# Kernel optimization log

Measured on AMD Instinct MI355X. Metric: run time of the kernel, lower is better.

## Reference

```python
import jax, jax.numpy as jnp
import numpy as np

C, N, NC, E, D, R = 16, 10000, 2000, 50000, 256, 32
NBLK = 3
IN_DIM = 4 + 134 + 6 * 4 + 18 * 4  # 234
EPS = 1e-5


def _instance_norm(x):
    # InstanceNorm1d (affine=False): normalize over the node axis per (config, channel)
    mu = jnp.mean(x, axis=1, keepdims=True)
    var = jnp.var(x, axis=1, keepdims=True)
    return (x - mu) * jax.lax.rsqrt(var + EPS)


def _channel_attn(x, W1, b1, W2, b2):
    t = jax.nn.relu(x @ W1 + b1)
    return jax.nn.sigmoid(t @ W2 + b2) * x


def setup_inputs() -> dict:
    key = jax.random.key(0)
    ks = jax.random.split(key, 24)
    sc = 0.05
    inp = {}
    inp["x_node_cfg"] = jax.random.randint(ks[0], (C, NC, 18), 0, 6)
    inp["x_feat"] = jax.random.normal(ks[1], (N, 134), jnp.float32)
    inp["x_node_layout_feat"] = jax.random.randint(ks[2], (N, 6), 0, 6)
    inp["x_op"] = jax.random.randint(ks[3], (N,), 0, 120)
    inp["edge_index"] = jax.random.randint(ks[4], (2, E), 0, N)
    inp["node_config_ids"] = jnp.arange(NC)
    # parameters
    inp["emb_op"] = jax.random.normal(ks[5], (120, 4)) * 0.1
    inp["emb_layout"] = jax.random.normal(ks[6], (8, 4)) * 0.1
    inp["lin1_W"] = jax.random.normal(ks[7], (IN_DIM, D)) * sc
    inp["lin1_b"] = jnp.full((D,), 0.01, jnp.float32)
    inp["ca1_W1"] = jax.random.normal(ks[8], (D, R)) * sc
    inp["ca1_b1"] = jnp.zeros((R,), jnp.float32)
    inp["ca1_W2"] = jax.random.normal(ks[9], (R, D)) * sc
    inp["ca1_b2"] = jnp.zeros((D,), jnp.float32)
    inp["lin2_W"] = jax.random.normal(ks[10], (D, D)) * sc
    inp["lin2_b"] = jnp.full((D,), 0.01, jnp.float32)
    inp["ca2_W1"] = jax.random.normal(ks[11], (D, R)) * sc
    inp["ca2_b1"] = jnp.zeros((R,), jnp.float32)
    inp["ca2_W2"] = jax.random.normal(ks[12], (R, D)) * sc
    inp["ca2_b2"] = jnp.zeros((D,), jnp.float32)
    inp["sage_Wl"] = jax.random.normal(ks[13], (NBLK, D, D)) * sc
    inp["sage_bl"] = jnp.zeros((NBLK, D), jnp.float32)
    inp["sage_Wr"] = jax.random.normal(ks[14], (NBLK, D, D)) * sc
    inp["sca_W1"] = jax.random.normal(ks[15], (NBLK, D, R)) * sc
    inp["sca_b1"] = jnp.zeros((NBLK, R), jnp.float32)
    inp["sca_W2"] = jax.random.normal(ks[16], (NBLK, R, D)) * sc
    inp["sca_b2"] = jnp.zeros((NBLK, D), jnp.float32)
    inp["cls_W"] = jax.random.normal(ks[17], (D, 1)) * sc
    inp["cls_b"] = jnp.zeros((1,), jnp.float32)
    return inp


def _forward(x_node_cfg, x_feat, x_node_layout_feat, x_op, edge_index, node_config_ids,
             emb_op, emb_layout, lin1_W, lin1_b, ca1_W1, ca1_b1, ca1_W2, ca1_b2,
             lin2_W, lin2_b, ca2_W1, ca2_b1, ca2_W2, ca2_b2,
             sage_Wl, sage_bl, sage_Wr, sca_W1, sca_b1, sca_W2, sca_b2, cls_W, cls_b):
    n_cfg = x_node_cfg.shape[0]
    n_nodes = x_feat.shape[0]
    # build per-node config feature: -2 fill, scatter configured nodes, shift by +2
    node_cfg = jnp.full((n_cfg, n_nodes, 18), -2, x_node_cfg.dtype)
    node_cfg = node_cfg.at[:, node_config_ids].set(x_node_cfg) + 2
    cfg_emb = emb_layout[node_cfg].reshape(n_cfg, n_nodes, 18 * 4)  # [C,N,72]
    layout_emb = emb_layout[x_node_layout_feat + 2].reshape(n_nodes, 6 * 4)  # [N,24]
    op_emb = emb_op[x_op]  # [N,4]
    feat = jnp.concatenate([
        jnp.broadcast_to(x_feat[None], (n_cfg, n_nodes, x_feat.shape[1])),
        cfg_emb,
        jnp.broadcast_to(layout_emb[None], (n_cfg, n_nodes, layout_emb.shape[1])),
        jnp.broadcast_to(op_emb[None], (n_cfg, n_nodes, op_emb.shape[1])),
    ], axis=2)  # [C,N,234]

    # LinearActNorm 1
    h = feat @ lin1_W + lin1_b
    h = _instance_norm(h)
    h = _channel_attn(h, ca1_W1, ca1_b1, ca1_W2, ca1_b2)
    h = jax.nn.gelu(h, approximate=False)
    # LinearActNorm 2
    h = h @ lin2_W + lin2_b
    h = _instance_norm(h)
    h = _channel_attn(h, ca2_W1, ca2_b1, ca2_W2, ca2_b2)
    h = jax.nn.gelu(h, approximate=False)

    src, tgt = edge_index[0], edge_index[1]
    cnt = jnp.zeros((n_nodes,), h.dtype).at[tgt].add(1.0)
    inv_cnt = (1.0 / jnp.maximum(cnt, 1.0))[None, :, None]
    for i in range(sage_Wl.shape[0]):
        shortcut = h
        x = _instance_norm(h)
        # SAGEConv: mean aggregation of source features at targets + root transform
        agg = jnp.zeros_like(x).at[:, tgt, :].add(x[:, src, :]) * inv_cnt
        x = agg @ sage_Wl[i] + sage_bl[i] + x @ sage_Wr[i]
        x = _channel_attn(x, sca_W1[i], sca_b1[i], sca_W2[i], sca_b2[i])
        h = jax.nn.gelu(x + shortcut, approximate=False)

    pooled = h.mean(axis=1)  # [C,D]
    return (pooled @ cls_W + cls_b).reshape(-1)  # [C]


def reference(x_node_cfg, x_feat, x_node_layout_feat, x_op, edge_index, node_config_ids,
              emb_op, emb_layout, lin1_W, lin1_b, ca1_W1, ca1_b1, ca1_W2, ca1_b2,
              lin2_W, lin2_b, ca2_W1, ca2_b1, ca2_W2, ca2_b2,
              sage_Wl, sage_bl, sage_Wr, sca_W1, sca_b1, sca_W2, sca_b2, cls_W, cls_b):
    return _forward(x_node_cfg, x_feat, x_node_layout_feat, x_op, edge_index, node_config_ids,
                    emb_op, emb_layout, lin1_W, lin1_b, ca1_W1, ca1_b1, ca1_W2, ca1_b2,
                    lin2_W, lin2_b, ca2_W1, ca2_b1, ca2_W2, ca2_b2,
                    sage_Wl, sage_bl, sage_Wr, sca_W1, sca_b1, sca_W2, sca_b2, cls_W, cls_b)
```

## Files before the change

### kernel.cpp

```cpp
#include <hip/hip_runtime.h>
#include <hip/hip_bf16.h>
#include <math.h>

constexpr int C_  = 16;
constexpr int N_  = 10000;
constexpr int NC_ = 2000;
constexpr int E_  = 50000;
constexpr int D_  = 256;
constexpr int SZ_ = N_ * D_;
constexpr float EPS_ = 1e-5f;

typedef unsigned short u16;
typedef __attribute__((ext_vector_type(8))) unsigned short us8v;
typedef __attribute__((ext_vector_type(4))) unsigned short us4v;
typedef __attribute__((ext_vector_type(8))) short s16x8;
typedef __attribute__((ext_vector_type(4))) float f32x4;

typedef __attribute__((address_space(3))) unsigned int lds_uint;
typedef const __attribute__((address_space(1))) unsigned int glb_uint;

__device__ __forceinline__ u16 f2bf(float f) {
    __hip_bfloat16 h = __float2bfloat16(f);
    return __builtin_bit_cast(u16, h);
}
__device__ __forceinline__ float bf2f(u16 h) {
    return __uint_as_float(((unsigned)h) << 16);
}
__device__ __forceinline__ float gelu_f(float x) {
    float z = x * 0.70710678118654752f;
    float az = fabsf(z);
    float t = 1.f / fmaf(0.3275911f, az, 1.f);
    float p = t * (0.254829592f + t * (-0.284496736f + t * (1.421413741f +
              t * (-1.453152027f + t * 1.061405429f))));
    float e = p * __expf(-z * z);
    float erfv = (z >= 0.f) ? (1.f - e) : (e - 1.f);
    return 0.5f * x * (1.f + erfv);
}


__global__ __launch_bounds__(256) void tbl_k(const float* __restrict__ embL,
                                             const float* __restrict__ W,
                                             float* __restrict__ T) {
    int b = blockIdx.x;
    int s = b >> 3, i = b & 7, d = threadIdx.x;
    float acc = 0.f;
#pragma unroll
    for (int k = 0; k < 4; ++k)
        acc = fmaf(embL[i * 4 + k], W[(134 + s * 4 + k) * 256 + d], acc);
    T[(s * 8 + i) * 256 + d] = acc;
}

__global__ __launch_bounds__(256) void csum_k(const float* __restrict__ T,
                                              float* __restrict__ cs) {
    int d = threadIdx.x;
    float a = 0.f;
#pragma unroll
    for (int s = 0; s < 18; ++s) a += T[(s * 8) * 256 + d];
    cs[d] = a;
}

__global__ __launch_bounds__(192) void feat_k(const float* __restrict__ xf,
                                              const int* __restrict__ xlay,
                                              const int* __restrict__ xop,
                                              const float* __restrict__ embL,
                                              const float* __restrict__ embO,
                                              float* __restrict__ f) {
    int n = blockIdx.x, j = threadIdx.x;
    if (j >= 176) return;
    float v;
    if (j < 134) v = xf[n * 134 + j];
    else if (j < 158) { int q = j - 134; int t = q >> 2, k = q & 3; v = embL[(xlay[n * 6 + t] + 2) * 4 + k]; }
    else if (j < 162) { int k = j - 158; v = embO[xop[n] * 4 + k]; }
    else v = 0.f;
    f[n * 176 + j] = v;
}

__global__ __launch_bounds__(256) void wpack_k(const float* __restrict__ W,
                                               float* __restrict__ Wp) {
    int j = blockIdx.x, d = threadIdx.x;
    float v = 0.f;
    if (j < 134) v = W[j * 256 + d];
    else if (j < 158) v = W[(206 + j - 134) * 256 + d];
    else if (j < 162) v = W[(230 + j - 158) * 256 + d];
    Wp[j * 256 + d] = v;
}

__global__ __launch_bounds__(256) void packw1_k(const float* __restrict__ W1,
                                                u16* __restrict__ dst) {
    int i = blockIdx.x * 256 + threadIdx.x;
    int j = i & 7, lane = (i >> 3) & 63, half = (i >> 9) & 1, ks = (i >> 10) & 1, wid = (i >> 11) & 3;
    int k = wid * 64 + ks * 32 + ((lane >> 4) << 3) + j;
    int col = half * 16 + (lane & 15);
    dst[i] = f2bf(W1[k * 32 + col]);
}
__global__ __launch_bounds__(256) void packw2_k(const float* __restrict__ W2,
                                                u16* __restrict__ dst) {
    int i = blockIdx.x * 256 + threadIdx.x;
    int j = i & 7, lane = (i >> 3) & 63, q = (i >> 9) & 3, wid = (i >> 11) & 3;
    int kq = lane >> 4, cl = lane & 15;
    dst[i] = f2bf(W2[(kq * 8 + j) * 256 + (wid * 4 + q) * 16 + cl]);
}

__global__ __launch_bounds__(256) void cfgpos_k(const int* __restrict__ ncid,
                                                int* __restrict__ cfgpos) {
    int i = blockIdx.x * 256 + threadIdx.x;
    if (i < NC_) cfgpos[ncid[i]] = i;
}

__global__ __launch_bounds__(256) void hist_k(const int* __restrict__ ei, int* __restrict__ cnt) {
    int e = blockIdx.x * 256 + threadIdx.x;
    if (e < E_) atomicAdd(&cnt[ei[E_ + e]], 1);
}

__global__ __launch_bounds__(1024) void scan_k(const int* __restrict__ cnt,
                                               int* __restrict__ off,
                                               int* __restrict__ cursor,
                                               float* __restrict__ invcnt) {
    __shared__ int s[1024];
    int t = threadIdx.x;
    int base = t * 10;
    int local[10];
    int part = 0;
#pragma unroll
    for (int k = 0; k < 10; ++k) {
        int idx = base + k;
        int v = (idx < N_) ? cnt[idx] : 0;
        local[k] = v; part += v;
    }
    s[t] = part;
    __syncthreads();
    for (int o = 1; o < 1024; o <<= 1) {
        int val = (t >= o) ? s[t - o] : 0;
        __syncthreads();
        s[t] += val;
        __syncthreads();
    }
    int pre = s[t] - part;
#pragma unroll
    for (int k = 0; k < 10; ++k) {
        int idx = base + k;
        if (idx < N_) {
            off[idx] = pre;
            cursor[idx] = pre;
            invcnt[idx] = 1.0f / (float)(local[k] > 1 ? local[k] : 1);
            pre += local[k];
        }
    }
    if (t == 1023) off[N_] = s[1023];
}

__global__ __launch_bounds__(256) void fill_k(const int* __restrict__ ei,
                                              int* __restrict__ cursor,
                                              int* __restrict__ csr) {
    int e = blockIdx.x * 256 + threadIdx.x;
    if (e < E_) {
        int t = ei[E_ + e];
        int p = atomicAdd(&cursor[t], 1);
        csr[p] = ei[e];
    }
}

__global__ __launch_bounds__(256) void wt2_k(const float* __restrict__ W,
                                             u16* __restrict__ Wt) {
    int j = blockIdx.x, k = threadIdx.x;
    Wt[j * 256 + k] = f2bf(W[k * 256 + j]);
}

__global__ __launch_bounds__(256) void foldw_k(const float* __restrict__ Wl,
                                               const float* __restrict__ Wr,
                                               const float* __restrict__ bl,
                                               const float* __restrict__ mu,
                                               const float* __restrict__ rs,
                                               u16* __restrict__ Wt,
                                               float* __restrict__ biasF) {
    __shared__ float red[256];
    int c = blockIdx.y, j = blockIdx.x, k = threadIdx.x;
    float rsv = rs[c * 256 + k], muv = mu[c * 256 + k];
    float fl = rsv * Wl[k * 256 + j];
    float fr = rsv * Wr[k * 256 + j];
    size_t wb = ((size_t)c * 256 + j) * 512;
    Wt[wb + k] = f2bf(fl);
    Wt[wb + 256 + k] = f2bf(fr);
    red[k] = muv * (fl + fr);
    __syncthreads();
    for (int s = 128; s > 0; s >>= 1) {
        if (k < s) red[k] += red[k + s];
        __syncthreads();
    }
    if (k == 0) biasF[c * 256 + j] = bl[j] - red[0];
}

__global__ __launch_bounds__(256) void lin1_cfg_k(const float* __restrict__ base,
                                                  const float* __restrict__ T,
                                                  const int* __restrict__ ncid,
                                                  const int* __restrict__ xcfg,
                                                  u16* __restrict__ H,
                                                  float* __restrict__ ssum,
                                                  float* __restrict__ ssq) {
    __shared__ int idxs[16][18];
    __shared__ int nid[16];
    const int c = blockIdx.z, j0 = blockIdx.x * 16, tid = threadIdx.x;
    if (tid < 16) nid[tid] = ncid[j0 + tid];
    for (int t = tid; t < 288; t += 256) {
        int row = t / 18, s = t - row * 18;
        idxs[row][s] = (xcfg[((size_t)c * NC_ + j0 + row) * 18 + s] + 2) * 256;
    }
    __syncthreads();
    const int d = tid;
    float psum = 0.f, psq = 0.f;
    for (int g = 0; g < 16; g += 4) {
        float acc[4];
#pragma unroll
        for (int gg = 0; gg < 4; ++gg) acc[gg] = base[(size_t)nid[g + gg] * 256 + d];
#pragma unroll
        for (int s = 0; s < 18; ++s) {
            const float* Ts = &T[s * 2048 + d];
#pragma unroll
            for (int gg = 0; gg < 4; ++gg)
                acc[gg] += Ts[idxs[g + gg][s]];
        }
#pragma unroll
        for (int gg = 0; gg < 4; ++gg) {
            H[((size_t)c * N_ + nid[g + gg]) * 256 + d] = f2bf(acc[gg]);
            psum += acc[gg]; psq += acc[gg] * acc[gg];
        }
    }
    atomicAdd(&ssum[c * 256 + d], psum);
    atomicAdd(&ssq[c * 256 + d], psq);
}

__global__ __launch_bounds__(256) void lin1_unc_k(const float* __restrict__ base,
                                                  const float* __restrict__ csum,
                                                  const int* __restrict__ cfgpos,
                                                  int nc,
                                                  u16* __restrict__ H,
                                                  float* __restrict__ ssum,
                                                  float* __restrict__ ssq) {
    __shared__ float red[2048];
    const int n0 = blockIdx.x * 16, tid = threadIdx.x;
    float ps[8] = {0, 0, 0, 0, 0, 0, 0, 0}, pq[8] = {0, 0, 0, 0, 0, 0, 0, 0};
#pragma unroll
    for (int it = 0; it < 2; ++it) {
        const int flat = tid + it * 256;
        const int row = flat >> 5, cb = (flat & 31) * 8;
        const int n = n0 + row;
        if (cfgpos[n] >= 0) continue;
        us8v b;
#pragma unroll
        for (int j = 0; j < 8; ++j) {
            float v = base[(size_t)n * 256 + cb + j] + csum[cb + j];
            b[j] = f2bf(v);
            ps[j] += v; pq[j] += v * v;
        }
        for (int c = 0; c < nc; ++c)
            *(us8v*)&H[((size_t)c * N_ + n) * 256 + cb] = b;
    }
#pragma unroll
    for (int j = 0; j < 8; ++j)
        red[((tid >> 5) * 32 + (tid & 31)) * 8 + j] = ps[j];
    __syncthreads();
    {
        const int cb2 = tid >> 3, j2 = tid & 7;
        float s = 0.f;
#pragma unroll
        for (int r8 = 0; r8 < 8; ++r8) s += red[(r8 * 32 + cb2) * 8 + j2];
        for (int c = 0; c < nc; ++c) atomicAdd(&ssum[c * 256 + tid], s);
    }
    __syncthreads();
#pragma unroll
    for (int j = 0; j < 8; ++j)
        red[((tid >> 5) * 32 + (tid & 31)) * 8 + j] = pq[j];
    __syncthreads();
    {
        const int cb2 = tid >> 3, j2 = tid & 7;
        float s = 0.f;
#pragma unroll
        for (int r8 = 0; r8 < 8; ++r8) s += red[(r8 * 32 + cb2) * 8 + j2];
        for (int c = 0; c < nc; ++c) atomicAdd(&ssq[c * 256 + tid], s);
    }
}

__global__ __launch_bounds__(256) void finstat_k(const float* __restrict__ ssum,
                                                 const float* __restrict__ ssq,
                                                 float* __restrict__ mu,
                                                 float* __restrict__ rs,
                                                 float* __restrict__ mrs) {
    int i = blockIdx.x * 256 + threadIdx.x;
    float m = ssum[i] * (1.0f / (float)N_);
    float v = ssq[i] * (1.0f / (float)N_) - m * m;
    float r = rsqrtf(v + EPS_);
    mu[i] = m;
    rs[i] = r;
    mrs[i] = m * r;
}

__global__ __launch_bounds__(256) void agg_k(const u16* __restrict__ H,
                                             const int* __restrict__ off,
                                             const int* __restrict__ csr,
                                             const float* __restrict__ invcnt,
                                             const float* __restrict__ mu,
                                             u16* __restrict__ Agg) {
    int wave = threadIdx.x >> 6, lane = threadIdx.x & 63;
    int pair = blockIdx.x * 4 + wave;
    int c = pair / N_, t = pair - c * N_;
    int d4 = lane * 4;
    int o0 = off[t], o1 = off[t + 1];
    int deg = o1 - o0;
    us4v o;
    if (deg > 0) {
        int myidx = (lane < deg) ? csr[o0 + lane] : 0;
        const u16* Hc = H + (size_t)c * SZ_ + d4;
        float ax = 0.f, ay = 0.f, az = 0.f, aw = 0.f;
        int lim = deg < 64 ? deg : 64;
        int i = 0;
        for (; i + 4 <= lim; i += 4) {
            int s0 = __shfl(myidx, i), s1 = __shfl(myidx, i + 1);
            int s2 = __shfl(myidx, i + 2), s3 = __shfl(myidx, i + 3);
            us4v h0 = *(const us4v*)&Hc[(size_t)s0 * 256];
            us4v h1 = *(const us4v*)&Hc[(size_t)s1 * 256];
            us4v h2 = *(const us4v*)&Hc[(size_t)s2 * 256];
            us4v h3 = *(const us4v*)&Hc[(size_t)s3 * 256];
            ax += (bf2f(h0.x) + bf2f(h1.x)) + (bf2f(h2.x) + bf2f(h3.x));
            ay += (bf2f(h0.y) + bf2f(h1.y)) + (bf2f(h2.y) + bf2f(h3.y));
            az += (bf2f(h0.z) + bf2f(h1.z)) + (bf2f(h2.z) + bf2f(h3.z));
            aw += (bf2f(h0.w) + bf2f(h1.w)) + (bf2f(h2.w) + bf2f(h3.w));
        }
        for (; i < lim; ++i) {
            int s = __shfl(myidx, i);
            us4v h = *(const us4v*)&Hc[(size_t)s * 256];
            ax += bf2f(h.x); ay += bf2f(h.y); az += bf2f(h.z); aw += bf2f(h.w);
        }
        for (int j = o0 + 64; j < o1; ++j) {
            int s = csr[j];
            us4v h = *(const us4v*)&Hc[(size_t)s * 256];
            ax += bf2f(h.x); ay += bf2f(h.y); az += bf2f(h.z); aw += bf2f(h.w);
        }
        float inv = invcnt[t];
        o.x = f2bf(ax * inv); o.y = f2bf(ay * inv);
        o.z = f2bf(az * inv); o.w = f2bf(aw * inv);
    } else {
        o.x = f2bf(mu[c * 256 + d4 + 0]);
        o.y = f2bf(mu[c * 256 + d4 + 1]);
        o.z = f2bf(mu[c * 256 + d4 + 2]);
        o.w = f2bf(mu[c * 256 + d4 + 3]);
    }
    *(us4v*)&Agg[((size_t)c * N_ + t) * 256 + d4] = o;
}

template <int STATS>
__global__ __launch_bounds__(256) void mgemm_k(
    const u16* __restrict__ A1, size_t sA1,
    const u16* __restrict__ A2, size_t sA2,
    const u16* __restrict__ Wt, size_t sW, int K1, int Ktot,
    const float* __restrict__ bias, size_t sBias,
    u16* __restrict__ Y, size_t sY, int Mrows,
    float* __restrict__ ssum, float* __restrict__ ssq)
{
    __shared__ u16 Asm[128 * 64];
    __shared__ u16 Bsm[128 * 64];
    const int tid = threadIdx.x;
    const int lane = tid & 63, wid = tid >> 6;
    const int wr = wid >> 1, wc = wid & 1;

    const int gx = gridDim.x, gy = gridDim.y;
    int nwg = gx * gy * gridDim.z;
    int orig = blockIdx.x + gx * (blockIdx.y + gy * blockIdx.z);
    int q = nwg >> 3, r = nwg & 7;
    int xcd = orig & 7, idx = orig >> 3;
    int swz = (xcd < r ? xcd * (q + 1) : r * (q + 1) + (xcd - r) * q) + idx;
    const int bx = swz % gx;
    const int tmp = swz / gx;
    const int by = tmp % gy;
    const int c  = tmp / gy;

    const int rowbase = by * 128, colbase = bx * 128;

    const u16* A1p = A1 + (size_t)c * sA1;
    const u16* A2p = A2 ? (A2 + (size_t)c * sA2) : nullptr;
    const u16* Wp  = Wt + (size_t)c * sW;

    f32x4 acc[4][4];
#pragma unroll
    for (int i = 0; i < 4; ++i)
#pragma unroll
        for (int j = 0; j < 4; ++j) acc[i][j] = (f32x4)0.f;

    const int lrow = lane >> 3;
    const int lchunk = lane & 7;

    for (int k0 = 0; k0 < Ktot; k0 += 64) {
        const u16* asrc; int ak;
        if (k0 < K1) { asrc = A1p; ak = k0; } else { asrc = A2p; ak = k0 - K1; }
#pragma unroll
        for (int i = 0; i < 4; ++i) {
            const int row = (wid * 4 + i) * 8 + lrow;
            const int srcchunk = lchunk ^ (row & 7);
            int garow = rowbase + row;
            if (garow >= Mrows) garow = Mrows - 1;
            const u16* ga = asrc + (size_t)garow * 256 + ak + srcchunk * 8;
            __builtin_amdgcn_global_load_lds((glb_uint*)ga,
                (lds_uint*)(Asm + (wid * 4 + i) * 512), 16, 0, 0);
            const u16* gb = Wp + (size_t)(colbase + row) * Ktot + k0 + srcchunk * 8;
            __builtin_amdgcn_global_load_lds((glb_uint*)gb,
                (lds_uint*)(Bsm + (wid * 4 + i) * 512), 16, 0, 0);
        }
        __syncthreads();
#pragma unroll
        for (int ks = 0; ks < 2; ++ks) {
            s16x8 aF[4], bF[4];
            const int kk = ks * 32 + ((lane >> 4) << 3);
#pragma unroll
            for (int f = 0; f < 4; ++f) {
                int ar = wr * 64 + f * 16 + (lane & 15);
                aF[f] = *(const s16x8*)&Asm[(ar * 64 + kk) ^ ((ar & 7) << 3)];
                int br = wc * 64 + f * 16 + (lane & 15);
                bF[f] = *(const s16x8*)&Bsm[(br * 64 + kk) ^ ((br & 7) << 3)];
            }
#pragma unroll
            for (int fr = 0; fr < 4; ++fr)
#pragma unroll
                for (int fc = 0; fc < 4; ++fc)
                    acc[fr][fc] = __builtin_amdgcn_mfma_f32_16x16x32_bf16(
                        aF[fr], bF[fc], acc[fr][fc], 0, 0, 0);
        }
        __syncthreads();
    }

    float bcol[4];
#pragma unroll
    for (int fc = 0; fc < 4; ++fc)
        bcol[fc] = bias[(size_t)c * sBias + colbase + wc * 64 + fc * 16 + (lane & 15)];
    u16* Yp = Y + (size_t)c * sY;
    float ps[4] = {0, 0, 0, 0}, pq[4] = {0, 0, 0, 0};
#pragma unroll
    for (int fr = 0; fr < 4; ++fr) {
#pragma unroll
        for (int i = 0; i < 4; ++i) {
            int grow = rowbase + wr * 64 + fr * 16 + ((lane >> 4) << 2) + i;
            if (grow < Mrows) {
                size_t rb = (size_t)grow * 256 + colbase + wc * 64 + (lane & 15);
#pragma unroll
                for (int fc = 0; fc < 4; ++fc) {
                    float v = acc[fr][fc][i] + bcol[fc];
                    Yp[rb + fc * 16] = f2bf(v);
                    if (STATS) { ps[fc] += v; pq[fc] += v * v; }
                }
            }
        }
    }
    if (STATS) {
#pragma unroll
        for (int fc = 0; fc < 4; ++fc) {
            float s = ps[fc], q2 = pq[fc];
            s += __shfl_xor(s, 16); s += __shfl_xor(s, 32);
            q2 += __shfl_xor(q2, 16); q2 += __shfl_xor(q2, 32);
            if (lane < 16) {
                int col = colbase + wc * 64 + fc * 16 + lane;
                atomicAdd(&ssum[c * 256 + col], s);
                atomicAdd(&ssq[c * 256 + col], q2);
            }
        }
    }
}

__global__ __launch_bounds__(256) void gemm_k(const float* __restrict__ A1, int lda1,
                                              const float* __restrict__ W1, int K1,
                                              const float* __restrict__ bias,
                                              float* __restrict__ Y, int Mrows) {
    __shared__ float As[16][132];
    __shared__ float Bs[16][132];
    float acc[8][8];
#pragma unroll
    for (int i = 0; i < 8; ++i)
#pragma unroll
        for (int j = 0; j < 8; ++j) acc[i][j] = 0.f;

    const int tid = threadIdx.x;
    const int tr = tid >> 4, tc = tid & 15;
    const int rowbase = blockIdx.y * 128, colbase = blockIdx.x * 128;

    for (int k0 = 0; k0 < K1; k0 += 16) {
#pragma unroll
        for (int ii = 0; ii < 2; ++ii) {
            int i = tid + ii * 256;
            int rr = i >> 2, qq = i & 3;
            int grow = rowbase + rr;
            float4 vv = make_float4(0.f, 0.f, 0.f, 0.f);
            if (grow < Mrows) vv = *(const float4*)&A1[(size_t)grow * lda1 + k0 + qq * 4];
            As[qq * 4 + 0][rr] = vv.x;
            As[qq * 4 + 1][rr] = vv.y;
            As[qq * 4 + 2][rr] = vv.z;
            As[qq * 4 + 3][rr] = vv.w;
        }
#pragma unroll
        for (int ii = 0; ii < 2; ++ii) {
            int i = tid + ii * 256;
            int rr = i >> 5, qq = i & 31;
            float4 vv = *(const float4*)&W1[(size_t)(k0 + rr) * 256 + colbase + qq * 4];
            *(float4*)&Bs[rr][qq * 4] = vv;
        }
        __syncthreads();
#pragma unroll
        for (int kk = 0; kk < 16; ++kk) {
            float a[8], b[8];
            *(float4*)&a[0] = *(const float4*)&As[kk][tr * 4];
            *(float4*)&a[4] = *(const float4*)&As[kk][64 + tr * 4];
            *(float4*)&b[0] = *(const float4*)&Bs[kk][tc * 4];
            *(float4*)&b[4] = *(const float4*)&Bs[kk][64 + tc * 4];
#pragma unroll
            for (int i = 0; i < 8; ++i)
#pragma unroll
                for (int j = 0; j < 8; ++j)
                    acc[i][j] = fmaf(a[i], b[j], acc[i][j]);
        }
        __syncthreads();
    }

    float4 blo = *(const float4*)&bias[colbase + tc * 4];
    float4 bhi = *(const float4*)&bias[colbase + 64 + tc * 4];
    float bb[8] = {blo.x, blo.y, blo.z, blo.w, bhi.x, bhi.y, bhi.z, bhi.w};
#pragma unroll
    for (int i = 0; i < 8; ++i)
#pragma unroll
        for (int j = 0; j < 8; ++j) acc[i][j] += bb[j];

#pragma unroll
    for (int i = 0; i < 8; ++i) {
        int lrow = (i < 4) ? (tr * 4 + i) : (64 + tr * 4 + (i - 4));
        int grow = rowbase + lrow;
        if (grow < Mrows) {
            *(float4*)&Y[(size_t)grow * 256 + colbase + tc * 4] =
                make_float4(acc[i][0], acc[i][1], acc[i][2], acc[i][3]);
            *(float4*)&Y[(size_t)grow * 256 + colbase + 64 + tc * 4] =
                make_float4(acc[i][4], acc[i][5], acc[i][6], acc[i][7]);
        }
    }
}

template <int NORM, int RES, int SMODE>
__global__ __launch_bounds__(512) void apply_k(const u16* __restrict__ Yin,
                                               u16* __restrict__ Hout,
                                               const u16* __restrict__ Hsc,
                                               const u16* __restrict__ W1p,
                                               const float* __restrict__ b1,
                                               const u16* __restrict__ W2p,
                                               const float* __restrict__ b2,
                                               const float* __restrict__ rs,
                                               const float* __restrict__ mrs,
                                               float* __restrict__ ssum,
                                               float* __restrict__ ssq) {
    __shared__ u16 vbf[16 * 264];
    __shared__ u16 scs[(RES ? 16 : 1) * 264];
    __shared__ float tpart[8 * 528];
    __shared__ u16 tbf[16 * 40];
    __shared__ float srs[NORM ? 256 : 1], smrs[NORM ? 256 : 1];
    const int c = blockIdx.z, n0 = blockIdx.x * 16, tid = threadIdx.x;
    const int lane = tid & 63, wid = tid >> 6;
    const size_t rowbase = ((size_t)c * N_ + n0) * 256;

    if (NORM && tid < 256) { srs[tid] = rs[c * 256 + tid]; smrs[tid] = mrs[c * 256 + tid]; }
    {
        const int row = tid >> 5, cb = (tid & 31) * 8;
        us8v x = *(const us8v*)&Yin[rowbase + row * 256 + cb];
        us8v r;
        if (RES) r = *(const us8v*)&Hsc[rowbase + row * 256 + cb];
        if (NORM) {
            __syncthreads();
            us8v y;
#pragma unroll
            for (int j = 0; j < 8; ++j)
                y[j] = f2bf(fmaf(bf2f(x[j]), srs[cb + j], -smrs[cb + j]));
            *(us8v*)&vbf[row * 264 + cb] = y;
        } else {
            *(us8v*)&vbf[row * 264 + cb] = x;
        }
        if (RES) *(us8v*)&scs[row * 264 + cb] = r;
    }
    __syncthreads();

    {
        const int arow = lane & 15, kq = lane >> 4;
        const int k = wid * 32 + kq * 8;
        s16x8 aF = *(const s16x8*)&vbf[arow * 264 + k];
        s16x8 bF0 = *(const s16x8*)&W1p[((wid * 2 + 0) * 64 + lane) * 8];
        s16x8 bF1 = *(const s16x8*)&W1p[((wid * 2 + 1) * 64 + lane) * 8];
        f32x4 at0 = __builtin_amdgcn_mfma_f32_16x16x32_bf16(aF, bF0, (f32x4)0.f, 0, 0, 0);
        f32x4 at1 = __builtin_amdgcn_mfma_f32_16x16x32_bf16(aF, bF1, (f32x4)0.f, 0, 0, 0);
#pragma unroll
        for (int i = 0; i < 4; ++i) {
            tpart[wid * 528 + (kq * 4 + i) * 33 + (lane & 15)] = at0[i];
            tpart[wid * 528 + (kq * 4 + i) * 33 + 16 + (lane & 15)] = at1[i];
        }
    }
    __syncthreads();

    {
        const int nr = tid >> 5, col = tid & 31;
        float s = b1[col];
#pragma unroll
        for (int w8 = 0; w8 < 8; ++w8)
            s += tpart[w8 * 528 + nr * 33 + col];
        tbf[nr * 40 + col] = f2bf(fmaxf(s, 0.f));
    }
    __syncthreads();

    {
        const int cl = lane & 15, kq = lane >> 4;
        s16x8 aF = *(const s16x8*)&tbf[cl * 40 + kq * 8];
        float ps[2] = {0, 0}, pq[2] = {0, 0};
#pragma unroll
        for (int q = 0; q < 2; ++q) {
            const int colb = (wid * 2 + q) * 16;
            s16x8 bF = *(const s16x8*)&W2p[((wid * 2 + q) * 64 + lane) * 8];
            f32x4 acc = __builtin_amdgcn_mfma_f32_16x16x32_bf16(aF, bF, (f32x4)0.f, 0, 0, 0);
            const float b2v = b2[colb + cl];
#pragma unroll
            for (int i = 0; i < 4; ++i) {
                const int row = kq * 4 + i;
                const int ea = row * 264 + colb + cl;
                float s = acc[i] + b2v;
                float sig = 1.0f / (1.0f + __expf(-s));
                float val = sig * bf2f(vbf[ea]);
                if (RES) val += bf2f(scs[ea]);
                val = gelu_f(val);
                vbf[ea] = f2bf(val);
                if (SMODE) { ps[q] += val; if (SMODE == 1) pq[q] += val * val; }
            }
        }
        if (SMODE) {
#pragma unroll
            for (int q = 0; q < 2; ++q) {
                float s = ps[q];
                s += __shfl_xor(s, 16); s += __shfl_xor(s, 32);
                if (SMODE == 1) {
                    float q2 = pq[q];
                    q2 += __shfl_xor(q2, 16); q2 += __shfl_xor(q2, 32);
                    if (lane < 16) atomicAdd(&ssq[c * 256 + (wid * 2 + q) * 16 + lane], q2);
                }
                if (lane < 16) atomicAdd(&ssum[c * 256 + (wid * 2 + q) * 16 + lane], s);
            }
        }
    }
    __syncthreads();

    {
        const int row = tid >> 5, cb = (tid & 31) * 8;
        us8v h = *(const us8v*)&vbf[row * 264 + cb];
        *(us8v*)&Hout[rowbase + row * 256 + cb] = h;
    }
}

__global__ __launch_bounds__(256) void cls_k(const float* __restrict__ pooled_sum,
                                             const float* __restrict__ clsW,
                                             const float* __restrict__ clsb,
                                             float* __restrict__ out) {
    __shared__ float red[256];
    int c = blockIdx.x, d = threadIdx.x;
    red[d] = pooled_sum[c * 256 + d] * (1.0f / (float)N_) * clsW[d];
    __syncthreads();
    for (int s = 128; s > 0; s >>= 1) {
        if (d < s) red[d] += red[d + s];
        __syncthreads();
    }
    if (d == 0) out[c] = red[0] + clsb[0];
}

static inline size_t alup(size_t x) { return (x + 255) & ~(size_t)255; }

extern "C" void kernel_launch(void* const* d_in, const int* in_sizes, int n_in,
                              void* d_out, int out_size, void* d_ws, size_t ws_size,
                              hipStream_t stream) {
    const int*   xcfg   = (const int*)d_in[0];
    const float* xfeat  = (const float*)d_in[1];
    const int*   xlay   = (const int*)d_in[2];
    const int*   xop    = (const int*)d_in[3];
    const int*   ei     = (const int*)d_in[4];
    const int*   ncid   = (const int*)d_in[5];
    const float* embO   = (const float*)d_in[6];
    const float* embL   = (const float*)d_in[7];
    const float* lin1W  = (const float*)d_in[8];
    const float* lin1b  = (const float*)d_in[9];
    const float* ca1W1  = (const float*)d_in[10];
    const float* ca1b1  = (const float*)d_in[11];
    const float* ca1W2  = (const float*)d_in[12];
    const float* ca1b2  = (const float*)d_in[13];
    const float* lin2W  = (const float*)d_in[14];
    const float* lin2b  = (const float*)d_in[15];
    const float* ca2W1  = (const float*)d_in[16];
    const float* ca2b1  = (const float*)d_in[17];
    const float* ca2W2  = (const float*)d_in[18];
    const float* ca2b2  = (const float*)d_in[19];
    const float* sageWl = (const float*)d_in[20];
    const float* sagebl = (const float*)d_in[21];
    const float* sageWr = (const float*)d_in[22];
    const float* scaW1  = (const float*)d_in[23];
    const float* scab1  = (const float*)d_in[24];
    const float* scaW2  = (const float*)d_in[25];
    const float* scab2  = (const float*)d_in[26];
    const float* clsW   = (const float*)d_in[27];
    const float* clsb   = (const float*)d_in[28];
    float* out = (float*)d_out;

    char* w = (char*)d_ws;
    size_t o = 0;
    auto take = [&](size_t bytes) { char* p = w + o; o = alup(o + bytes); return p; };
    float* base    = (float*)take((size_t)N_ * 256 * 4);
    float* feat162 = (float*)take((size_t)N_ * 176 * 4);
    float* W162    = (float*)take((size_t)176 * 256 * 4);
    float* T       = (float*)take((size_t)18 * 8 * 256 * 4);
    float* csum    = (float*)take((size_t)256 * 4);
    float* stats   = (float*)take((size_t)6 * 8192 * 4);
    float* MU      = (float*)take((size_t)5 * 4096 * 4);
    float* RS      = (float*)take((size_t)5 * 4096 * 4);
    float* MRS     = (float*)take((size_t)5 * 4096 * 4);
    float* invcnt  = (float*)take((size_t)N_ * 4);
    int*   cnt     = (int*)take((size_t)N_ * 4);
    int*   off     = (int*)take((size_t)(N_ + 1) * 4);
    int*   cursor  = (int*)take((size_t)N_ * 4);
    int*   csr     = (int*)take((size_t)E_ * 4);
    int*   cfgpos  = (int*)take((size_t)N_ * 4);
    u16*   Wt2     = (u16*)take((size_t)256 * 256 * 2);
    u16*   Wfold   = (u16*)take((size_t)C_ * 256 * 512 * 2);
    float* biasF   = (float*)take((size_t)C_ * 256 * 4);
    u16*   CAW1    = (u16*)take((size_t)5 * 8192 * 2);
    u16*   CAW2    = (u16*)take((size_t)5 * 8192 * 2);

    const size_t slab = (size_t)SZ_ * 2;
    size_t avail = (ws_size > o) ? (ws_size - o) : 0;
    int Cc = (int)(avail / (3 * slab + 768));
    if (Cc > C_) Cc = C_;
    if (Cc < 1) Cc = 1;
    u16* BufH = (u16*)take((size_t)Cc * slab);
    u16* BufY = (u16*)take((size_t)Cc * slab);
    u16* BufA = (u16*)take((size_t)Cc * slab);
    (void)in_sizes; (void)n_in; (void)out_size;

    auto S = [&](int s) { return stats + (size_t)s * 8192; };
    auto Q = [&](int s) { return stats + (size_t)s * 8192 + 4096; };

    hipMemsetAsync(stats, 0, 6 * 8192 * 4, stream);
    hipMemsetAsync(cnt, 0, N_ * 4, stream);
    hipMemsetAsync(cfgpos, 0xFF, N_ * 4, stream);

    tbl_k<<<144, 256, 0, stream>>>(embL, lin1W, T);
    csum_k<<<1, 256, 0, stream>>>(T, csum);
    feat_k<<<N_, 192, 0, stream>>>(xfeat, xlay, xop, embL, embO, feat162);
    wpack_k<<<176, 256, 0, stream>>>(lin1W, W162);
    wt2_k<<<256, 256, 0, stream>>>(lin2W, Wt2);
    packw1_k<<<32, 256, 0, stream>>>(ca1W1, CAW1 + 0 * 8192);
    packw1_k<<<32, 256, 0, stream>>>(ca2W1, CAW1 + 1 * 8192);
    packw1_k<<<32, 256, 0, stream>>>(scaW1 + 0 * 8192, CAW1 + 2 * 8192);
    packw1_k<<<32, 256, 0, stream>>>(scaW1 + 1 * 8192, CAW1 + 3 * 8192);
    packw1_k<<<32, 256, 0, stream>>>(scaW1 + 2 * 8192, CAW1 + 4 * 8192);
    packw2_k<<<32, 256, 0, stream>>>(ca1W2, CAW2 + 0 * 8192);
    packw2_k<<<32, 256, 0, stream>>>(ca2W2, CAW2 + 1 * 8192);
    packw2_k<<<32, 256, 0, stream>>>(scaW2 + 0 * 8192, CAW2 + 2 * 8192);
    packw2_k<<<32, 256, 0, stream>>>(scaW2 + 1 * 8192, CAW2 + 3 * 8192);
    packw2_k<<<32, 256, 0, stream>>>(scaW2 + 2 * 8192, CAW2 + 4 * 8192);
    cfgpos_k<<<(NC_ + 255) / 256, 256, 0, stream>>>(ncid, cfgpos);
    hist_k<<<(E_ + 255) / 256, 256, 0, stream>>>(ei, cnt);
    scan_k<<<1, 1024, 0, stream>>>(cnt, off, cursor, invcnt);
    fill_k<<<(E_ + 255) / 256, 256, 0, stream>>>(ei, cursor, csr);

    gemm_k<<<dim3(2, 79, 1), 256, 0, stream>>>(feat162, 176, W162, 176, lin1b, base, N_);

    for (int c0 = 0; c0 < C_; c0 += Cc) {
        const int nc = (C_ - c0 < Cc) ? (C_ - c0) : Cc;
        const int co = c0 * 256;

        lin1_cfg_k<<<dim3(NC_ / 16, 1, nc), 256, 0, stream>>>(
            base, T, ncid, xcfg + (size_t)c0 * NC_ * 18, BufH, S(0) + co, Q(0) + co);
        lin1_unc_k<<<625, 256, 0, stream>>>(
            base, csum, cfgpos, nc, BufH, S(0) + co, Q(0) + co);
        finstat_k<<<nc, 256, 0, stream>>>(S(0) + co, Q(0) + co,
                                          MU + co, RS + co, MRS + co);

        apply_k<1, 0, 0><<<dim3(625, 1, nc), 512, 0, stream>>>(
            BufH, BufH, nullptr, CAW1 + 0 * 8192, ca1b1, CAW2 + 0 * 8192, ca1b2,
            RS + co, MRS + co, nullptr, nullptr);

        mgemm_k<1><<<dim3(2, 79, nc), 256, 0, stream>>>(
            BufH, SZ_, nullptr, 0, Wt2, 0, 256, 256,
            lin2b, 0, BufY, SZ_, N_, S(1) + co, Q(1) + co);
        finstat_k<<<nc, 256, 0, stream>>>(S(1) + co, Q(1) + co,
                                          MU + 4096 + co, RS + 4096 + co, MRS + 4096 + co);

        apply_k<1, 0, 1><<<dim3(625, 1, nc), 512, 0, stream>>>(
            BufY, BufY, nullptr, CAW1 + 1 * 8192, ca2b1, CAW2 + 1 * 8192, ca2b2,
            RS + 4096 + co, MRS + 4096 + co, S(2) + co, Q(2) + co);

        for (int i = 0; i < 3; ++i) {
            const int set = 2 + i;
            finstat_k<<<nc, 256, 0, stream>>>(S(set) + co, Q(set) + co,
                                              MU + set * 4096 + co, RS + set * 4096 + co,
                                              MRS + set * 4096 + co);
            foldw_k<<<dim3(256, nc), 256, 0, stream>>>(
                sageWl + (size_t)i * 65536, sageWr + (size_t)i * 65536, sagebl + i * 256,
                MU + set * 4096 + co, RS + set * 4096 + co,
                Wfold + (size_t)c0 * 256 * 512, biasF + co);
            agg_k<<<nc * 2500, 256, 0, stream>>>(BufY, off, csr, invcnt,
                                                 MU + set * 4096 + co, BufA);
            mgemm_k<0><<<dim3(2, 79, nc), 256, 0, stream>>>(
                BufA, SZ_, BufY, SZ_, Wfold + (size_t)c0 * 256 * 512, 256 * 512, 256, 512,
                biasF + co, 256, BufH, SZ_, N_, nullptr, nullptr);
            if (i < 2) {
                apply_k<0, 1, 1><<<dim3(625, 1, nc), 512, 0, stream>>>(
                    BufH, BufY, BufY,
                    CAW1 + (2 + i) * 8192, scab1 + i * 32,
                    CAW2 + (2 + i) * 8192, scab2 + i * 256,
                    nullptr, nullptr, S(3 + i) + co, Q(3 + i) + co);
            } else {
                apply_k<0, 1, 2><<<dim3(625, 1, nc), 512, 0, stream>>>(
                    BufH, BufY, BufY,
                    CAW1 + (2 + i) * 8192, scab1 + i * 32,
                    CAW2 + (2 + i) * 8192, scab2 + i * 256,
                    nullptr, nullptr, S(5) + co, nullptr);
            }
        }
    }

    cls_k<<<16, 256, 0, stream>>>(S(5), clsW, clsb, out);
}
```

Measured before the change: 1.359 ms.

## Fuse SAGE GEMM with channel attention, residual GELU and stats

Replaces the separate folded SAGE GEMM and apply kernel with a single kernel. It computes a full 128x256 output tile per workgroup, then runs channel attention, the residual GELU and the column statistics on that tile in LDS. This removes the BufH intermediate write and read and one launch per block. In exchange the GEMM runs with fewer, larger workgroups (79 x configs), uses heavy LDS, and has no K-loop pipelining, which may lower occupancy.

```diff
diff --git a/kernel.cpp b/kernel.cpp
--- a/kernel.cpp
+++ b/kernel.cpp
@@ -458,6 +458,216 @@
                 int col = colbase + wc * 64 + fc * 16 + lane;
                 atomicAdd(&ssum[c * 256 + col], s);
                 atomicAdd(&ssq[c * 256 + col], q2);
+            }
+        }
+    }
+}
+
+template <int SMODE>
+__global__ __launch_bounds__(512) void msage_k(
+    const u16* __restrict__ A1,
+    const u16* __restrict__ A2,
+    const u16* __restrict__ Wt, size_t sW,
+    const float* __restrict__ biasF,
+    const u16* __restrict__ W1p, const float* __restrict__ b1,
+    const u16* __restrict__ W2p, const float* __restrict__ b2,
+    u16* __restrict__ Yout, int Mrows,
+    float* __restrict__ ssum, float* __restrict__ ssq)
+{
+    __shared__ __align__(16) char SM[56320];
+    u16*   Asm   = (u16*)SM;
+    u16*   Bsm   = (u16*)(SM + 16384);
+    u16*   xbf   = (u16*)SM;
+    float* tpart = (float*)(SM + 33792);
+    u16*   tbf   = (u16*)(SM + 50688);
+    float* red   = tpart;
+
+    const int tid = threadIdx.x;
+    const int lane = tid & 63, wid = tid >> 6;
+    const int wr = wid >> 2, wc = wid & 3;
+    const int cl = lane & 15, kq = lane >> 4;
+
+    int nwg = gridDim.x * gridDim.y;
+    int orig = blockIdx.x + gridDim.x * blockIdx.y;
+    int q = nwg >> 3, r = nwg & 7;
+    int xcd = orig & 7, idx = orig >> 3;
+    int swz = (xcd < r ? xcd * (q + 1) : r * (q + 1) + (xcd - r) * q) + idx;
+    const int by = swz % gridDim.x;
+    const int c  = swz / gridDim.x;
+    const int rowbase = by * 128;
+
+    const u16* A1p = A1 + (size_t)c * SZ_;
+    const u16* A2p = A2 + (size_t)c * SZ_;
+    const u16* Wp  = Wt + (size_t)c * sW;
+
+    f32x4 acc[4][4];
+#pragma unroll
+    for (int i = 0; i < 4; ++i)
+#pragma unroll
+        for (int j = 0; j < 4; ++j) acc[i][j] = (f32x4)0.f;
+
+    for (int k0 = 0; k0 < 512; k0 += 64) {
+        const u16* asrc = (k0 < 256) ? A1p : A2p;
+        const int ak = (k0 < 256) ? k0 : (k0 - 256);
+#pragma unroll
+        for (int jj = 0; jj < 2; ++jj) {
+            const int u = tid + jj * 512;
+            const int row = u >> 3, chunk = u & 7;
+            const int sc2 = chunk ^ (row & 7);
+            int garow = rowbase + row;
+            if (garow >= Mrows) garow = Mrows - 1;
+            __builtin_amdgcn_global_load_lds(
+                (glb_uint*)(asrc + (size_t)garow * 256 + ak + sc2 * 8),
+                (lds_uint*)(Asm + (jj * 512 + wid * 64) * 8), 16, 0, 0);
+        }
+#pragma unroll
+        for (int jj = 0; jj < 4; ++jj) {
+            const int u = tid + jj * 512;
+            const int wcol = u >> 3, chunk = u & 7;
+            const int sc2 = chunk ^ (wcol & 7);
+            __builtin_amdgcn_global_load_lds(
+                (glb_uint*)(Wp + (size_t)wcol * 512 + k0 + sc2 * 8),
+                (lds_uint*)(Bsm + (jj * 512 + wid * 64) * 8), 16, 0, 0);
+        }
+        __syncthreads();
+#pragma unroll
+        for (int ks = 0; ks < 2; ++ks) {
+            s16x8 aF[4], bF[4];
+            const int kk = ks * 32 + kq * 8;
+#pragma unroll
+            for (int f = 0; f < 4; ++f) {
+                const int ar = wr * 64 + f * 16 + cl;
+                aF[f] = *(const s16x8*)&Asm[(ar * 64 + kk) ^ ((ar & 7) << 3)];
+                const int bc = wc * 64 + f * 16 + cl;
+                bF[f] = *(const s16x8*)&Bsm[(bc * 64 + kk) ^ ((bc & 7) << 3)];
+            }
+#pragma unroll
+            for (int fr = 0; fr < 4; ++fr)
+#pragma unroll
+                for (int fc = 0; fc < 4; ++fc)
+                    acc[fr][fc] = __builtin_amdgcn_mfma_f32_16x16x32_bf16(
+                        aF[fr], bF[fc], acc[fr][fc], 0, 0, 0);
+        }
+        __syncthreads();
+    }
+
+    float bcol[4];
+#pragma unroll
+    for (int fc = 0; fc < 4; ++fc)
+        bcol[fc] = biasF[c * 256 + wc * 64 + fc * 16 + cl];
+
+    for (int h = 0; h < 2; ++h) {
+        __syncthreads();
+        if (wr == h) {
+#pragma unroll
+            for (int fr = 0; fr < 4; ++fr)
+#pragma unroll
+                for (int i = 0; i < 4; ++i) {
+                    const int rloc = fr * 16 + kq * 4 + i;
+#pragma unroll
+                    for (int fc = 0; fc < 4; ++fc)
+                        xbf[rloc * 264 + wc * 64 + fc * 16 + cl] =
+                            f2bf(acc[fr][fc][i] + bcol[fc]);
+                }
+        }
+        __syncthreads();
+        {
+            const int rb = wid >> 1, kh = wid & 1;
+            f32x4 at0 = (f32x4)0.f, at1 = (f32x4)0.f;
+#pragma unroll
+            for (int ks = 0; ks < 4; ++ks) {
+                const int s = kh * 4 + ks;
+                s16x8 aF = *(const s16x8*)&xbf[(rb * 16 + cl) * 264 + s * 32 + kq * 8];
+                s16x8 bF0 = *(const s16x8*)&W1p[((s * 2 + 0) * 64 + lane) * 8];
+                s16x8 bF1 = *(const s16x8*)&W1p[((s * 2 + 1) * 64 + lane) * 8];
+                at0 = __builtin_amdgcn_mfma_f32_16x16x32_bf16(aF, bF0, at0, 0, 0, 0);
+                at1 = __builtin_amdgcn_mfma_f32_16x16x32_bf16(aF, bF1, at1, 0, 0, 0);
+            }
+#pragma unroll
+            for (int i = 0; i < 4; ++i) {
+                tpart[(rb * 2 + kh) * 528 + (kq * 4 + i) * 33 + cl] = at0[i];
+                tpart[(rb * 2 + kh) * 528 + (kq * 4 + i) * 33 + 16 + cl] = at1[i];
+            }
+        }
+        __syncthreads();
+#pragma unroll
+        for (int it = 0; it < 4; ++it) {
+            const int e = tid + it * 512;
+            const int row = e >> 5, col = e & 31;
+            const int rb = row >> 4, rr = row & 15;
+            float s = tpart[(rb * 2) * 528 + rr * 33 + col] +
+                      tpart[(rb * 2 + 1) * 528 + rr * 33 + col] + b1[col];
+            tbf[row * 40 + col] = f2bf(fmaxf(s, 0.f));
+        }
+        __syncthreads();
+        {
+            s16x8 aF[4];
+#pragma unroll
+            for (int rg = 0; rg < 4; ++rg)
+                aF[rg] = *(const s16x8*)&tbf[(rg * 16 + cl) * 40 + kq * 8];
+#pragma unroll
+            for (int q2 = 0; q2 < 2; ++q2) {
+                const int colb = (wid * 2 + q2) * 16;
+                s16x8 bF = *(const s16x8*)&W2p[((wid * 2 + q2) * 64 + lane) * 8];
+                const float b2v = b2[colb + cl];
+#pragma unroll
+                for (int rg = 0; rg < 4; ++rg) {
+                    f32x4 a2 = __builtin_amdgcn_mfma_f32_16x16x32_bf16(
+                        aF[rg], bF, (f32x4)0.f, 0, 0, 0);
+#pragma unroll
+                    for (int i = 0; i < 4; ++i) {
+                        const int ea = (rg * 16 + kq * 4 + i) * 264 + colb + cl;
+                        float s = a2[i] + b2v;
+                        float sig = 1.f / (1.f + __expf(-s));
+                        xbf[ea] = f2bf(sig * bf2f(xbf[ea]));
+                    }
+                }
+            }
+        }
+        __syncthreads();
+        float ps[8] = {0, 0, 0, 0, 0, 0, 0, 0}, pq[8] = {0, 0, 0, 0, 0, 0, 0, 0};
+#pragma unroll
+        for (int it = 0; it < 4; ++it) {
+            const int e = tid + it * 512;
+            const int row = e >> 5, cb = (e & 31) * 8;
+            const int grow = rowbase + h * 64 + row;
+            if (grow < Mrows) {
+                us8v xv = *(const us8v*)&xbf[row * 264 + cb];
+                us8v rv = *(const us8v*)&Yout[((size_t)c * N_ + grow) * 256 + cb];
+                us8v ov;
+#pragma unroll
+                for (int j = 0; j < 8; ++j) {
+                    float v = gelu_f(bf2f(xv[j]) + bf2f(rv[j]));
+                    ov[j] = f2bf(v);
+                    ps[j] += v;
+                    if (SMODE == 1) pq[j] += v * v;
+                }
+                *(us8v*)&Yout[((size_t)c * N_ + grow) * 256 + cb] = ov;
+            }
+        }
+#pragma unroll
+        for (int j = 0; j < 8; ++j)
+            red[((tid >> 5) * 32 + (tid & 31)) * 8 + j] = ps[j];
+        __syncthreads();
+        if (tid < 256) {
+            const int cb2 = tid >> 3, j2 = tid & 7;
+            float s = 0.f;
+#pragma unroll
+            for (int r16 = 0; r16 < 16; ++r16) s += red[(r16 * 32 + cb2) * 8 + j2];
+            atomicAdd(&ssum[c * 256 + cb2 * 8 + j2], s);
+        }
+        if (SMODE == 1) {
+            __syncthreads();
+#pragma unroll
+            for (int j = 0; j < 8; ++j)
+                red[((tid >> 5) * 32 + (tid & 31)) * 8 + j] = pq[j];
+            __syncthreads();
+            if (tid < 256) {
+                const int cb2 = tid >> 3, j2 = tid & 7;
+                float s = 0.f;
+#pragma unroll
+                for (int r16 = 0; r16 < 16; ++r16) s += red[(r16 * 32 + cb2) * 8 + j2];
+                atomicAdd(&ssq[c * 256 + cb2 * 8 + j2], s);
             }
         }
     }
@@ -800,21 +1010,18 @@
                 Wfold + (size_t)c0 * 256 * 512, biasF + co);
             agg_k<<<nc * 2500, 256, 0, stream>>>(BufY, off, csr, invcnt,
                                                  MU + set * 4096 + co, BufA);
-            mgemm_k<0><<<dim3(2, 79, nc), 256, 0, stream>>>(
-                BufA, SZ_, BufY, SZ_, Wfold + (size_t)c0 * 256 * 512, 256 * 512, 256, 512,
-                biasF + co, 256, BufH, SZ_, N_, nullptr, nullptr);
             if (i < 2) {
-                apply_k<0, 1, 1><<<dim3(625, 1, nc), 512, 0, stream>>>(
-                    BufH, BufY, BufY,
+                msage_k<1><<<dim3(79, nc), 512, 0, stream>>>(
+                    BufA, BufY, Wfold + (size_t)c0 * 256 * 512, 256 * 512, biasF + co,
                     CAW1 + (2 + i) * 8192, scab1 + i * 32,
                     CAW2 + (2 + i) * 8192, scab2 + i * 256,
-                    nullptr, nullptr, S(3 + i) + co, Q(3 + i) + co);
+                    BufY, N_, S(3 + i) + co, Q(3 + i) + co);
             } else {
-                apply_k<0, 1, 2><<<dim3(625, 1, nc), 512, 0, stream>>>(
-                    BufH, BufY, BufY,
+                msage_k<2><<<dim3(79, nc), 512, 0, stream>>>(
+                    BufA, BufY, Wfold + (size_t)c0 * 256 * 512, 256 * 512, biasF + co,
                     CAW1 + (2 + i) * 8192, scab1 + i * 32,
                     CAW2 + (2 + i) * 8192, scab2 + i * 256,
-                    nullptr, nullptr, S(5) + co, nullptr);
+                    BufY, N_, S(5) + co, nullptr);
             }
         }
     }
```

After: 1.307 ms. 3.8% less time.
